# Performance work log

Hardware: AMD Instinct MI355X
Metric: run time of the kernel (lower is better)

The kernel has to match this reference:

```python
import jax, jax.numpy as jnp
import numpy as np

B, T, F = 2048, 96, 32
H = 1024
G_EMB = 16
LSTM_IN = F + 11 + 1 + G_EMB  # 60


def _lstm_cell(x, h, c, W_ih, W_hh, b):
    g = x @ W_ih.T + h @ W_hh.T + b
    i, f, gg, o = jnp.split(g, 4, axis=-1)  # torch gate order: i, f, g, o
    c_new = jax.nn.sigmoid(f) * c + jax.nn.sigmoid(i) * jnp.tanh(gg)
    h_new = jax.nn.sigmoid(o) * jnp.tanh(c_new)
    return h_new, c_new


def setup_inputs() -> dict:
    key = jax.random.key(0)
    ks = jax.random.split(key, 26)
    s = 1.0 / np.sqrt(H)
    inp = {
        "dec_known": jax.random.normal(ks[0], (B, T, F), jnp.float32),
        "target_y": jax.random.normal(ks[1], (B, T, 1), jnp.float32),
        "enc_h": jax.random.normal(ks[2], (2, B, H), jnp.float32),
        "enc_c": jax.random.normal(ks[3], (2, B, H), jnp.float32),
        "last_enc_consumption": jax.random.normal(ks[4], (B, 1), jnp.float32),
        "group_ids": jax.random.randint(ks[5], (B,), 0, 1000),
        "cat_province": jax.random.randint(ks[6], (B,), 0, 13),
        "cat_customer_type": jax.random.randint(ks[7], (B,), 0, 2),
        "cat_price_type": jax.random.randint(ks[8], (B,), 0, 5),
        "cat_consumption_level": jax.random.randint(ks[9], (B,), 0, 3),
        # learned parameters
        "group_emb": jax.random.normal(ks[10], (1000, G_EMB), jnp.float32),
        "emb_province": jax.random.normal(ks[11], (13, 4), jnp.float32),
        "emb_customer_type": jax.random.normal(ks[12], (2, 2), jnp.float32),
        "emb_price_type": jax.random.normal(ks[13], (5, 3), jnp.float32),
        "emb_consumption_level": jax.random.normal(ks[14], (3, 2), jnp.float32),
        "W_ih0": jax.random.normal(ks[15], (4 * H, LSTM_IN), jnp.float32) * s,
        "W_hh0": jax.random.normal(ks[16], (4 * H, H), jnp.float32) * s,
        "b0": jax.random.normal(ks[17], (4 * H,), jnp.float32) * s,
        "W_ih1": jax.random.normal(ks[18], (4 * H, H), jnp.float32) * s,
        "W_hh1": jax.random.normal(ks[19], (4 * H, H), jnp.float32) * s,
        "b1": jax.random.normal(ks[20], (4 * H,), jnp.float32) * s,
        "W_proj": jax.random.normal(ks[21], (1, H), jnp.float32) * s,
        "b_proj": jnp.zeros((1,), jnp.float32),
    }
    return inp


def reference(dec_known, target_y, enc_h, enc_c, last_enc_consumption,
              group_ids, cat_province, cat_customer_type, cat_price_type,
              cat_consumption_level, group_emb, emb_province, emb_customer_type,
              emb_price_type, emb_consumption_level, W_ih0, W_hh0, b0,
              W_ih1, W_hh1, b1, W_proj, b_proj):
    b, t, _ = dec_known.shape
    # static per-sample features (categorical + group embeddings)
    cat_emb = jnp.concatenate([
        emb_province[cat_province], emb_customer_type[cat_customer_type],
        emb_price_type[cat_price_type], emb_consumption_level[cat_consumption_level],
    ], axis=-1)  # [B, 11]
    group_vec = group_emb[group_ids]  # [B, 16]
    static = jnp.concatenate([cat_emb, group_vec], axis=-1)  # [B, 27]
    # teacher_forcing_ratio = 1.0 => prev_y is last_enc_consumption then target_y shifted
    prev_y = jnp.concatenate([last_enc_consumption[:, None, :], target_y[:, :-1, :]], axis=1)  # [B,T,1]
    x = jnp.concatenate([
        prev_y, dec_known,
        jnp.broadcast_to(static[:, None, :], (b, t, static.shape[-1])),
    ], axis=-1)  # [B, T, 60]

    def step(carry, x_t):
        h1, c1, h2, c2 = carry
        h1, c1 = _lstm_cell(x_t, h1, c1, W_ih0, W_hh0, b0)
        h2, c2 = _lstm_cell(h1, h2, c2, W_ih1, W_hh1, b1)
        return (h1, c1, h2, c2), h2

    init = (enc_h[0], enc_c[0], enc_h[1], enc_c[1])
    _, hs = jax.lax.scan(step, init, jnp.swapaxes(x, 0, 1))  # hs: [T, B, H]
    y = jnp.einsum('tbh,oh->bto', hs, W_proj) + b_proj  # [B, T, 1]
    return y
```

## Files before the change

### kernel.cpp

```cpp
#include <hip/hip_runtime.h>
#include <hip/hip_bf16.h>
#include <stdint.h>


#define BB  2048
#define TT  96
#define NG  4096
#define KL1 1088
#define KL2 2048

typedef __bf16 bf16;
typedef __bf16 bf16x8 __attribute__((ext_vector_type(8)));
typedef float  f32x4  __attribute__((ext_vector_type(4)));

__device__ __forceinline__ float sigm(float x) { return 1.0f / (1.0f + __expf(-x)); }

__device__ __forceinline__ void gload16(const bf16* g, bf16* l) {
  __builtin_amdgcn_global_load_lds((const __attribute__((address_space(1))) void*)g,
                                   (__attribute__((address_space(3))) void*)l, 16, 0, 0);
}


__global__ __launch_bounds__(256) void build_w0(const float* __restrict__ Wih0,
                                                const float* __restrict__ Whh0,
                                                bf16* __restrict__ W0) {
  int idx = blockIdx.x * 256 + threadIdx.x;
  if (idx >= NG * KL1) return;
  int np = idx / KL1, k = idx % KL1;
  int n = (np & 3) * 1024 + (np >> 2);
  float v;
  if (k < 60)       v = Wih0[n * 60 + k];
  else if (k < 64)  v = 0.0f;
  else              v = Whh0[n * 1024 + (k - 64)];
  W0[idx] = (bf16)v;
}

__global__ __launch_bounds__(256) void build_w1(const float* __restrict__ Wih1,
                                                const float* __restrict__ Whh1,
                                                bf16* __restrict__ W1) {
  int idx = blockIdx.x * 256 + threadIdx.x;
  if (idx >= NG * KL2) return;
  int np = idx >> 11, k = idx & 2047;
  int n = (np & 3) * 1024 + (np >> 2);
  float v = (k < 1024) ? Wih1[n * 1024 + k] : Whh1[n * 1024 + (k - 1024)];
  W1[idx] = (bf16)v;
}

__global__ __launch_bounds__(256) void perm_bias(const float* __restrict__ b0,
                                                 const float* __restrict__ b1,
                                                 float* __restrict__ b0p,
                                                 float* __restrict__ b1p) {
  int idx = blockIdx.x * 256 + threadIdx.x;
  if (idx >= NG) return;
  int n = (idx & 3) * 1024 + (idx >> 2);
  b0p[idx] = b0[n];
  b1p[idx] = b1[n];
}

__global__ __launch_bounds__(256) void build_x(
    const float* __restrict__ dec, const float* __restrict__ ty, const float* __restrict__ lec,
    const int* __restrict__ gid, const int* __restrict__ cp, const int* __restrict__ cct,
    const int* __restrict__ cpt, const int* __restrict__ ccl,
    const float* __restrict__ gemb, const float* __restrict__ ep, const float* __restrict__ ect,
    const float* __restrict__ ept, const float* __restrict__ ecl,
    bf16* __restrict__ X) {
  int idx = blockIdx.x * 256 + threadIdx.x;
  if (idx >= BB * TT) return;
  int b = idx / TT, t = idx % TT;
  bf16* x = X + (size_t)idx * 64;
  x[0] = (bf16)((t == 0) ? lec[b] : ty[b * TT + t - 1]);
  const float* d = dec + (size_t)idx * 32;
  #pragma unroll
  for (int k = 0; k < 32; ++k) x[1 + k] = (bf16)d[k];
  const float* e;
  e = ep  + cp[b]  * 4;  for (int j = 0; j < 4;  ++j) x[33 + j] = (bf16)e[j];
  e = ect + cct[b] * 2;  for (int j = 0; j < 2;  ++j) x[37 + j] = (bf16)e[j];
  e = ept + cpt[b] * 3;  for (int j = 0; j < 3;  ++j) x[39 + j] = (bf16)e[j];
  e = ecl + ccl[b] * 2;  for (int j = 0; j < 2;  ++j) x[42 + j] = (bf16)e[j];
  e = gemb + gid[b] * 16; for (int j = 0; j < 16; ++j) x[44 + j] = (bf16)e[j];
  for (int j = 60; j < 64; ++j) x[j] = (bf16)0.0f;
}

__global__ __launch_bounds__(256) void init_state(const float* __restrict__ enc_h,
                                                  const float* __restrict__ enc_c,
                                                  bf16* __restrict__ H1b,
                                                  bf16* __restrict__ H2b,
                                                  float* __restrict__ c1t,
                                                  float* __restrict__ c2t) {
  int idx = blockIdx.x * 256 + threadIdx.x;
  if (idx >= BB * 1024) return;
  int b = idx >> 10, h = idx & 1023;
  H1b[idx] = (bf16)enc_h[idx];
  H2b[idx] = (bf16)enc_h[(size_t)BB * 1024 + idx];
  c1t[(size_t)h * BB + b] = enc_c[idx];
  c2t[(size_t)h * BB + b] = enc_c[(size_t)BB * 1024 + idx];
}


template <int MODE>
__device__ __forceinline__ void gemm_cell_body(
    int vb, int t,
    const bf16* __restrict__ P0, const bf16* __restrict__ P1,
    const bf16* __restrict__ Wt, const float* __restrict__ bperm,
    float* __restrict__ ct, bf16* __restrict__ Hout,
    const float* __restrict__ wp, const float* __restrict__ bp,
    float* __restrict__ y,
    bf16* As, bf16* Ws) {
  constexpr int KT = (MODE == 0) ? KL1 : KL2;
  constexpr int NT = KT / 32;

  int tid = threadIdx.x;
  int swz = (vb & 7) * 64 + (vb >> 3);
  int tm = (swz & 15) << 7;
  int tn = (swz >> 4) << 7;
  int lane = tid & 63;
  int w = tid >> 6;
  int wg = (w & 1) << 6;
  int wb = (w >> 1) << 6;

  f32x4 acc[4][4];
  #pragma unroll
  for (int mw = 0; mw < 4; ++mw)
    #pragma unroll
    for (int nb = 0; nb < 4; ++nb) acc[mw][nb] = (f32x4){0.f, 0.f, 0.f, 0.f};

  int r0 = tid >> 2, r1 = (256 + tid) >> 2;
  int kc0 = (((tid & 3) ^ (r0 & 3)) << 3);
  int kc1 = (((tid & 3) ^ (r1 & 3)) << 3);
  int dst0 = (tid & ~63) * 8;
  int dst1 = 2048 + dst0;

  auto aptr = [&](int row, int gk) -> const bf16* {
    if constexpr (MODE == 0) {
      return (gk < 64) ? (P0 + ((size_t)(tm + row) * TT + t) * 64 + gk)
                       : (P1 + (size_t)(tm + row) * 1024 + (gk - 64));
    } else {
      return (gk < 1024) ? (P0 + (size_t)(tm + row) * 1024 + gk)
                         : (P1 + (size_t)(tm + row) * 1024 + (gk - 1024));
    }
  };

  gload16(aptr(r0, kc0), As + dst0);
  gload16(aptr(r1, kc1), As + dst1);
  gload16(Wt + (size_t)(tn + r0) * KT + kc0, Ws + dst0);
  gload16(Wt + (size_t)(tn + r1) * KT + kc1, Ws + dst1);
  __syncthreads();

  int lrow = lane & 15;
  int klocal = (((lane >> 4) ^ (lane & 3)) << 3);

  for (int kt = 0; kt < NT; ++kt) {
    int cur = (kt & 1) << 12;
    if (kt + 1 < NT) {
      int nxt = 4096 - cur;
      int gk0 = (kt + 1) * 32 + kc0, gk1 = (kt + 1) * 32 + kc1;
      gload16(aptr(r0, gk0), As + nxt + dst0);
      gload16(aptr(r1, gk1), As + nxt + dst1);
      gload16(Wt + (size_t)(tn + r0) * KT + gk0, Ws + nxt + dst0);
      gload16(Wt + (size_t)(tn + r1) * KT + gk1, Ws + nxt + dst1);
    }
    __builtin_amdgcn_sched_barrier(0);

    bf16x8 af[4], wf[4];
    #pragma unroll
    for (int nb = 0; nb < 4; ++nb)
      af[nb] = *reinterpret_cast<const bf16x8*>(&As[cur + (wb + nb * 16 + lrow) * 32 + klocal]);
    #pragma unroll
    for (int mw = 0; mw < 4; ++mw)
      wf[mw] = *reinterpret_cast<const bf16x8*>(&Ws[cur + (wg + mw * 16 + lrow) * 32 + klocal]);
    #pragma unroll
    for (int mw = 0; mw < 4; ++mw)
      #pragma unroll
      for (int nb = 0; nb < 4; ++nb)
        acc[mw][nb] = __builtin_amdgcn_mfma_f32_16x16x32_bf16(wf[mw], af[nb], acc[mw][nb], 0, 0, 0);

    __syncthreads();
  }

  bf16* hst = As + w * 1024;
  int u = lane >> 4;
  int bl = lane & 15;
  int hwave = (tn + wg) >> 2;
  float yp[4] = {0.f, 0.f, 0.f, 0.f};

  #pragma unroll
  for (int mw = 0; mw < 4; ++mw) {
    int hg = hwave + mw * 4 + u;
    f32x4 bv = *reinterpret_cast<const f32x4*>(&bperm[hg * 4]);
    float wph = 0.f;
    if constexpr (MODE == 1) wph = wp[hg];
    #pragma unroll
    for (int nb = 0; nb < 4; ++nb) {
      int bg = tm + wb + nb * 16 + bl;
      float gi = acc[mw][nb][0] + bv[0];
      float gf = acc[mw][nb][1] + bv[1];
      float gg = acc[mw][nb][2] + bv[2];
      float go = acc[mw][nb][3] + bv[3];
      float* cp_ = ct + (size_t)hg * BB + bg;
      float c = *cp_;
      float cn = sigm(gf) * c + sigm(gi) * tanhf(gg);
      float hn = sigm(go) * tanhf(cn);
      *cp_ = cn;
      hst[(nb * 16 + bl) * 16 + mw * 4 + u] = (bf16)hn;
      if constexpr (MODE == 1) yp[nb] += hn * wph;
    }
  }

  asm volatile("s_waitcnt lgkmcnt(0)" ::: "memory");
  __builtin_amdgcn_sched_barrier(0);

  #pragma unroll
  for (int q = 0; q < 2; ++q) {
    int chunk = q * 64 + lane;
    int bl2 = chunk >> 1, half = chunk & 1;
    bf16x8 v = *reinterpret_cast<const bf16x8*>(&hst[bl2 * 16 + half * 8]);
    int bg = tm + wb + bl2;
    *reinterpret_cast<bf16x8*>(&Hout[(size_t)bg * 1024 + hwave + half * 8]) = v;
  }

  if constexpr (MODE == 1) {
    #pragma unroll
    for (int nb = 0; nb < 4; ++nb) {
      float s = yp[nb];
      s += __shfl_xor(s, 16);
      s += __shfl_xor(s, 32);
      if (lane < 16)
        atomicAdd(&y[(size_t)(tm + wb + nb * 16 + lane) * TT + t], s);
    }
  } else {
    if (tn == 0 && tid < 128) y[(size_t)(tm + tid) * TT + t] = bp[0];
  }
}

__global__ __launch_bounds__(256, 4) void step_kernel(
    const bf16* __restrict__ H1in, const bf16* __restrict__ H2in,
    bf16* __restrict__ H1out, bf16* __restrict__ H2out,
    const bf16* __restrict__ X,
    const bf16* __restrict__ W0, const bf16* __restrict__ W1,
    const float* __restrict__ b0p, const float* __restrict__ b1p,
    float* __restrict__ c1t, float* __restrict__ c2t,
    const float* __restrict__ wp, const float* __restrict__ bp,
    float* __restrict__ y, int t2, int only_l1) {
  __shared__ alignas(16) bf16 As[2 * 4096];
  __shared__ alignas(16) bf16 Ws[2 * 4096];
  int bid = (int)blockIdx.x;
  if (only_l1 || bid >= 512) {
    int vb = only_l1 ? bid : bid - 512;
    int t1 = t2 + 1;
    if (t1 >= TT) return;
    gemm_cell_body<0>(vb, t1, X, H1in, W0, b0p, c1t, H1out, nullptr, bp, y, As, Ws);
  } else {
    gemm_cell_body<1>(bid, t2, H1in, H2in, W1, b1p, c2t, H2out, wp, nullptr, y, As, Ws);
  }
}


extern "C" void kernel_launch(void* const* d_in, const int* in_sizes, int n_in,
                              void* d_out, int out_size, void* d_ws, size_t ws_size,
                              hipStream_t stream) {
  const float* dec   = (const float*)d_in[0];
  const float* ty    = (const float*)d_in[1];
  const float* enc_h = (const float*)d_in[2];
  const float* enc_c = (const float*)d_in[3];
  const float* lec   = (const float*)d_in[4];
  const int*   gid   = (const int*)d_in[5];
  const int*   cp    = (const int*)d_in[6];
  const int*   cct   = (const int*)d_in[7];
  const int*   cpt   = (const int*)d_in[8];
  const int*   ccl   = (const int*)d_in[9];
  const float* gemb  = (const float*)d_in[10];
  const float* ep    = (const float*)d_in[11];
  const float* ect   = (const float*)d_in[12];
  const float* ept   = (const float*)d_in[13];
  const float* ecl   = (const float*)d_in[14];
  const float* Wih0  = (const float*)d_in[15];
  const float* Whh0  = (const float*)d_in[16];
  const float* b0    = (const float*)d_in[17];
  const float* Wih1  = (const float*)d_in[18];
  const float* Whh1  = (const float*)d_in[19];
  const float* b1    = (const float*)d_in[20];
  const float* wp    = (const float*)d_in[21];
  const float* bp    = (const float*)d_in[22];
  float* y = (float*)d_out;

  char* ws = (char*)d_ws;
  bf16* W0    = (bf16*)ws;  ws += (size_t)NG * KL1 * 2;
  bf16* W1    = (bf16*)ws;  ws += (size_t)NG * KL2 * 2;
  bf16* X     = (bf16*)ws;  ws += (size_t)BB * TT * 64 * 2;
  bf16* H1a   = (bf16*)ws;  ws += (size_t)BB * 1024 * 2;
  bf16* H1b   = (bf16*)ws;  ws += (size_t)BB * 1024 * 2;
  bf16* H2a   = (bf16*)ws;  ws += (size_t)BB * 1024 * 2;
  bf16* H2b   = (bf16*)ws;  ws += (size_t)BB * 1024 * 2;
  float* c1t  = (float*)ws; ws += (size_t)BB * 1024 * 4;
  float* c2t  = (float*)ws; ws += (size_t)BB * 1024 * 4;
  float* b0p  = (float*)ws; ws += (size_t)NG * 4;
  float* b1p  = (float*)ws; ws += (size_t)NG * 4;

  build_w0<<<(NG * KL1 + 255) / 256, 256, 0, stream>>>(Wih0, Whh0, W0);
  build_w1<<<(NG * KL2 + 255) / 256, 256, 0, stream>>>(Wih1, Whh1, W1);
  perm_bias<<<NG / 256, 256, 0, stream>>>(b0, b1, b0p, b1p);
  build_x<<<(BB * TT + 255) / 256, 256, 0, stream>>>(dec, ty, lec, gid, cp, cct, cpt, ccl,
                                                     gemb, ep, ect, ept, ecl, X);
  init_state<<<(BB * 1024) / 256, 256, 0, stream>>>(enc_h, enc_c, H1b, H2b, c1t, c2t);

  step_kernel<<<512, 256, 0, stream>>>(H1b, nullptr, H1a, nullptr, X, W0, W1,
                                       b0p, b1p, c1t, c2t, wp, bp, y, -1, 1);
  for (int t = 0; t < TT; ++t) {
    bf16* h1i = (t & 1) ? H1b : H1a;
    bf16* h1o = (t & 1) ? H1a : H1b;
    bf16* h2i = (t & 1) ? H2a : H2b;
    bf16* h2o = (t & 1) ? H2b : H2a;
    step_kernel<<<1024, 256, 0, stream>>>(h1i, h2i, h1o, h2o, X, W0, W1,
                                          b0p, b1p, c1t, c2t, wp, bp, y, t, 0);
  }
}
```

Before: 7.137 ms.

## Prefetch two K-tiles ahead with explicit waitcnt barriers and new LDS swizzle

Restructures the GEMM main loop so that global-to-LDS loads for tile kt+2 are issued right after the current tile's fragments are read into registers. Synchronisation uses manual vmcnt/lgkmcnt waits and raw barriers, which gives loads a deeper prefetch distance and drops the trailing __syncthreads. The LDS XOR swizzle now keys on row>>1, to cut bank conflicts for the 16-row fragment reads. MFMA sections run at raised wave priority. This adds fragile hand-coded wait counts that must match the number of outstanding loads.

Result: no change. 7.236 ms (+1.4%).

```diff
diff --git a/kernel.cpp b/kernel.cpp
--- a/kernel.cpp
+++ b/kernel.cpp
@@ -125,8 +125,8 @@
     for (int nb = 0; nb < 4; ++nb) acc[mw][nb] = (f32x4){0.f, 0.f, 0.f, 0.f};
 
   int r0 = tid >> 2, r1 = (256 + tid) >> 2;
-  int kc0 = (((tid & 3) ^ (r0 & 3)) << 3);
-  int kc1 = (((tid & 3) ^ (r1 & 3)) << 3);
+  int kc0 = (((tid & 3) ^ ((r0 >> 1) & 3)) << 3);
+  int kc1 = (((tid & 3) ^ ((r1 >> 1) & 3)) << 3);
   int dst0 = (tid & ~63) * 8;
   int dst1 = 2048 + dst0;
 
@@ -139,26 +139,25 @@
                          : (P1 + (size_t)(tm + row) * 1024 + (gk - 1024));
     }
   };
-
-  gload16(aptr(r0, kc0), As + dst0);
-  gload16(aptr(r1, kc1), As + dst1);
-  gload16(Wt + (size_t)(tn + r0) * KT + kc0, Ws + dst0);
-  gload16(Wt + (size_t)(tn + r1) * KT + kc1, Ws + dst1);
-  __syncthreads();
+  auto stage = [&](int kt, int off) {
+    int gk0 = kt * 32 + kc0, gk1 = kt * 32 + kc1;
+    gload16(aptr(r0, gk0), As + off + dst0);
+    gload16(aptr(r1, gk1), As + off + dst1);
+    gload16(Wt + (size_t)(tn + r0) * KT + gk0, Ws + off + dst0);
+    gload16(Wt + (size_t)(tn + r1) * KT + gk1, Ws + off + dst1);
+  };
+
+  stage(0, 0);
+  stage(1, 4096);
 
   int lrow = lane & 15;
-  int klocal = (((lane >> 4) ^ (lane & 3)) << 3);
+  int klocal = ((((lane >> 4) ^ (lrow >> 1)) & 3) << 3);
 
   for (int kt = 0; kt < NT; ++kt) {
     int cur = (kt & 1) << 12;
-    if (kt + 1 < NT) {
-      int nxt = 4096 - cur;
-      int gk0 = (kt + 1) * 32 + kc0, gk1 = (kt + 1) * 32 + kc1;
-      gload16(aptr(r0, gk0), As + nxt + dst0);
-      gload16(aptr(r1, gk1), As + nxt + dst1);
-      gload16(Wt + (size_t)(tn + r0) * KT + gk0, Ws + nxt + dst0);
-      gload16(Wt + (size_t)(tn + r1) * KT + gk1, Ws + nxt + dst1);
-    }
+    if (kt + 1 < NT) { asm volatile("s_waitcnt vmcnt(4)" ::: "memory"); }
+    else             { asm volatile("s_waitcnt vmcnt(0)" ::: "memory"); }
+    __builtin_amdgcn_s_barrier();
     __builtin_amdgcn_sched_barrier(0);
 
     bf16x8 af[4], wf[4];
@@ -168,13 +167,21 @@
     #pragma unroll
     for (int mw = 0; mw < 4; ++mw)
       wf[mw] = *reinterpret_cast<const bf16x8*>(&Ws[cur + (wg + mw * 16 + lrow) * 32 + klocal]);
+
+    asm volatile("s_waitcnt lgkmcnt(0)" ::: "memory");
+    __builtin_amdgcn_sched_barrier(0);
+    __builtin_amdgcn_s_barrier();
+    __builtin_amdgcn_sched_barrier(0);
+
+    if (kt + 2 < NT) stage(kt + 2, cur);
+
+    __builtin_amdgcn_s_setprio(1);
     #pragma unroll
     for (int mw = 0; mw < 4; ++mw)
       #pragma unroll
       for (int nb = 0; nb < 4; ++nb)
         acc[mw][nb] = __builtin_amdgcn_mfma_f32_16x16x32_bf16(wf[mw], af[nb], acc[mw][nb], 0, 0, 0);
-
-    __syncthreads();
+    __builtin_amdgcn_s_setprio(0);
   }
 
   bf16* hst = As + w * 1024;
```

## Switch LSTM step GEMM to 256x256 tiles with 8-wave ping-pong pipeline

Applied to the files above, without the earlier changes.

Replaces the 128x128 tile, 4-wave step kernel with a 256x256 tile, 512-thread kernel using BK=64, double-buffered LDS staging interleaved with MFMA phases under explicit barriers and priority hints. X is re-laid out time-major so each step reads a contiguous slice, and block-to-tile mapping interleaves layer-1 and layer-2 tiles. Larger tiles raise arithmetic intensity and cut global traffic. The cost is only 256 blocks per step, which may underfill the 256 CUs, plus higher register pressure from 32 accumulators per lane.

Result: slower. 7.856 ms (+10.1%).

```diff
diff --git a/kernel.cpp b/kernel.cpp
--- a/kernel.cpp
+++ b/kernel.cpp
@@ -19,6 +19,11 @@
   __builtin_amdgcn_global_load_lds((const __attribute__((address_space(1))) void*)g,
                                    (__attribute__((address_space(3))) void*)l, 16, 0, 0);
 }
+
+#define SB()  __builtin_amdgcn_sched_barrier(0)
+#define BAR() __builtin_amdgcn_s_barrier()
+#define WAITV0() asm volatile("s_waitcnt vmcnt(0)" ::: "memory")
+#define WAITL0() asm volatile("s_waitcnt lgkmcnt(0)" ::: "memory")
 
 
 __global__ __launch_bounds__(256) void build_w0(const float* __restrict__ Wih0,
@@ -57,19 +62,19 @@
   b1p[idx] = b1[n];
 }
 
-__global__ __launch_bounds__(256) void build_x(
+__global__ __launch_bounds__(256) void build_x2(
     const float* __restrict__ dec, const float* __restrict__ ty, const float* __restrict__ lec,
     const int* __restrict__ gid, const int* __restrict__ cp, const int* __restrict__ cct,
     const int* __restrict__ cpt, const int* __restrict__ ccl,
     const float* __restrict__ gemb, const float* __restrict__ ep, const float* __restrict__ ect,
     const float* __restrict__ ept, const float* __restrict__ ecl,
-    bf16* __restrict__ X) {
+    bf16* __restrict__ X2) {
   int idx = blockIdx.x * 256 + threadIdx.x;
   if (idx >= BB * TT) return;
-  int b = idx / TT, t = idx % TT;
-  bf16* x = X + (size_t)idx * 64;
+  int t = idx >> 11, b = idx & 2047;
+  bf16* x = X2 + (size_t)idx * 64;
   x[0] = (bf16)((t == 0) ? lec[b] : ty[b * TT + t - 1]);
-  const float* d = dec + (size_t)idx * 32;
+  const float* d = dec + ((size_t)b * TT + t) * 32;
   #pragma unroll
   for (int k = 0; k < 32; ++k) x[1 + k] = (bf16)d[k];
   const float* e;
@@ -98,159 +103,216 @@
 
 
 template <int MODE>
-__device__ __forceinline__ void gemm_cell_body(
-    int vb, int t,
+__device__ __forceinline__ void gemm_body(
+    int tm, int tn, int t,
     const bf16* __restrict__ P0, const bf16* __restrict__ P1,
     const bf16* __restrict__ Wt, const float* __restrict__ bperm,
     float* __restrict__ ct, bf16* __restrict__ Hout,
     const float* __restrict__ wp, const float* __restrict__ bp,
     float* __restrict__ y,
-    bf16* As, bf16* Ws) {
+    bf16* Al, bf16* Wl)
+{
   constexpr int KT = (MODE == 0) ? KL1 : KL2;
-  constexpr int NT = KT / 32;
-
-  int tid = threadIdx.x;
-  int swz = (vb & 7) * 64 + (vb >> 3);
-  int tm = (swz & 15) << 7;
-  int tn = (swz >> 4) << 7;
-  int lane = tid & 63;
-  int w = tid >> 6;
-  int wg = (w & 1) << 6;
-  int wb = (w >> 1) << 6;
-
-  f32x4 acc[4][4];
+  constexpr int NT = KT / 64;
+
+  const int tid = threadIdx.x;
+  const int lane = tid & 63, w = tid >> 6;
+  const int l15 = lane & 15, u = lane >> 4;
+  const int wq = w & 3, wbh = w >> 2;
+
+  f32x4 acc[8][4];
   #pragma unroll
-  for (int mw = 0; mw < 4; ++mw)
-    #pragma unroll
-    for (int nb = 0; nb < 4; ++nb) acc[mw][nb] = (f32x4){0.f, 0.f, 0.f, 0.f};
-
-  int r0 = tid >> 2, r1 = (256 + tid) >> 2;
-  int kc0 = (((tid & 3) ^ (r0 & 3)) << 3);
-  int kc1 = (((tid & 3) ^ (r1 & 3)) << 3);
-  int dst0 = (tid & ~63) * 8;
-  int dst1 = 2048 + dst0;
-
-  auto aptr = [&](int row, int gk) -> const bf16* {
+  for (int i = 0; i < 8; ++i)
+    #pragma unroll
+    for (int j = 0; j < 4; ++j) acc[i][j] = (f32x4){0.f, 0.f, 0.f, 0.f};
+
+  const int srow = w * 8 + (lane >> 3);
+  const int kx   = (lane & 7) ^ (srow & 7);
+  const int dA   = w * 512 + lane * 8;
+  const int jx0 = ((u     ) ^ (l15 & 7)) << 3;
+  const int jx1 = ((4 + u ) ^ (l15 & 7)) << 3;
+
+  auto asrc = [&](int row, int kt) -> const bf16* {
     if constexpr (MODE == 0) {
-      return (gk < 64) ? (P0 + ((size_t)(tm + row) * TT + t) * 64 + gk)
-                       : (P1 + (size_t)(tm + row) * 1024 + (gk - 64));
+      if (kt == 0) return P0 + (size_t)(tm + row) * 64 + kx * 8;
+      return P1 + (size_t)(tm + row) * 1024 + (kt - 1) * 64 + kx * 8;
     } else {
-      return (gk < 1024) ? (P0 + (size_t)(tm + row) * 1024 + gk)
-                         : (P1 + (size_t)(tm + row) * 1024 + (gk - 1024));
+      if (kt < 16) return P0 + (size_t)(tm + row) * 1024 + kt * 64 + kx * 8;
+      return P1 + (size_t)(tm + row) * 1024 + (kt - 16) * 64 + kx * 8;
     }
   };
-
-  gload16(aptr(r0, kc0), As + dst0);
-  gload16(aptr(r1, kc1), As + dst1);
-  gload16(Wt + (size_t)(tn + r0) * KT + kc0, Ws + dst0);
-  gload16(Wt + (size_t)(tn + r1) * KT + kc1, Ws + dst1);
-  __syncthreads();
-
-  int lrow = lane & 15;
-  int klocal = (((lane >> 4) ^ (lane & 3)) << 3);
+  auto stageA = [&](int buf, int half, int kt) {
+    bf16* base = Al + (buf * 2 + half) * 8192;
+    gload16(asrc(half * 128 + srow, kt),      base + dA);
+    gload16(asrc(half * 128 + srow + 64, kt), base + dA + 4096);
+  };
+  auto stageW = [&](int buf, int half, int kt) {
+    bf16* base = Wl + (buf * 2 + half) * 8192;
+    const bf16* g0 = Wt + (size_t)(tn + half * 128 + srow) * KT + kt * 64 + kx * 8;
+    const bf16* g1 = Wt + (size_t)(tn + half * 128 + srow + 64) * KT + kt * 64 + kx * 8;
+    gload16(g0, base + dA);
+    gload16(g1, base + dA + 4096);
+  };
+  auto rdA = [&](int buf, int bf, int ks) -> bf16x8 {
+    return *reinterpret_cast<const bf16x8*>(
+        Al + (buf * 2 + wbh) * 8192 + (bf * 16 + l15) * 64 + (ks ? jx1 : jx0));
+  };
+  auto rdW = [&](int buf, int gf, int ks) -> bf16x8 {
+    return *reinterpret_cast<const bf16x8*>(
+        Wl + (buf * 2 + (wq >> 1)) * 8192 + ((wq & 1) * 64 + gf * 16 + l15) * 64 + (ks ? jx1 : jx0));
+  };
+
+  stageA(0, 0, 0); stageA(0, 1, 0); stageW(0, 0, 0); stageW(0, 1, 0);
+
+  bf16x8 a_[8], w0_[4], w1_[4];
 
   for (int kt = 0; kt < NT; ++kt) {
-    int cur = (kt & 1) << 12;
-    if (kt + 1 < NT) {
-      int nxt = 4096 - cur;
-      int gk0 = (kt + 1) * 32 + kc0, gk1 = (kt + 1) * 32 + kc1;
-      gload16(aptr(r0, gk0), As + nxt + dst0);
-      gload16(aptr(r1, gk1), As + nxt + dst1);
-      gload16(Wt + (size_t)(tn + r0) * KT + gk0, Ws + nxt + dst0);
-      gload16(Wt + (size_t)(tn + r1) * KT + gk1, Ws + nxt + dst1);
-    }
-    __builtin_amdgcn_sched_barrier(0);
-
-    bf16x8 af[4], wf[4];
-    #pragma unroll
-    for (int nb = 0; nb < 4; ++nb)
-      af[nb] = *reinterpret_cast<const bf16x8*>(&As[cur + (wb + nb * 16 + lrow) * 32 + klocal]);
-    #pragma unroll
-    for (int mw = 0; mw < 4; ++mw)
-      wf[mw] = *reinterpret_cast<const bf16x8*>(&Ws[cur + (wg + mw * 16 + lrow) * 32 + klocal]);
-    #pragma unroll
-    for (int mw = 0; mw < 4; ++mw)
+    const int buf = kt & 1, nbuf = buf ^ 1;
+    const bool pre = (kt + 1 < NT);
+
+    WAITV0(); SB(); BAR(); SB();
+    if (pre) { stageA(nbuf, 0, kt + 1); stageA(nbuf, 1, kt + 1); }
+
+    #pragma unroll
+    for (int bf = 0; bf < 4; ++bf) { a_[bf * 2] = rdA(buf, bf, 0); a_[bf * 2 + 1] = rdA(buf, bf, 1); }
+    #pragma unroll
+    for (int g = 0; g < 2; ++g) { w0_[g * 2] = rdW(buf, g, 0); w0_[g * 2 + 1] = rdW(buf, g, 1); }
+    if (pre) stageW(nbuf, 0, kt + 1);
+    SB(); BAR();
+    WAITL0(); SB();
+    __builtin_amdgcn_s_setprio(1);
+    #pragma unroll
+    for (int bf = 0; bf < 4; ++bf)
       #pragma unroll
-      for (int nb = 0; nb < 4; ++nb)
-        acc[mw][nb] = __builtin_amdgcn_mfma_f32_16x16x32_bf16(wf[mw], af[nb], acc[mw][nb], 0, 0, 0);
-
-    __syncthreads();
-  }
-
-  bf16* hst = As + w * 1024;
-  int u = lane >> 4;
-  int bl = lane & 15;
-  int hwave = (tn + wg) >> 2;
-  float yp[4] = {0.f, 0.f, 0.f, 0.f};
+      for (int g = 0; g < 2; ++g)
+        #pragma unroll
+        for (int ks = 0; ks < 2; ++ks)
+          acc[bf][g] = __builtin_amdgcn_mfma_f32_16x16x32_bf16(w0_[g * 2 + ks], a_[bf * 2 + ks], acc[bf][g], 0, 0, 0);
+    __builtin_amdgcn_s_setprio(0);
+    SB(); BAR();
+
+    #pragma unroll
+    for (int g = 0; g < 2; ++g) { w1_[g * 2] = rdW(buf, 2 + g, 0); w1_[g * 2 + 1] = rdW(buf, 2 + g, 1); }
+    if (pre) stageW(nbuf, 1, kt + 1);
+    SB(); BAR();
+    WAITL0(); SB();
+    __builtin_amdgcn_s_setprio(1);
+    #pragma unroll
+    for (int bf = 0; bf < 4; ++bf)
+      #pragma unroll
+      for (int g = 0; g < 2; ++g)
+        #pragma unroll
+        for (int ks = 0; ks < 2; ++ks)
+          acc[bf][2 + g] = __builtin_amdgcn_mfma_f32_16x16x32_bf16(w1_[g * 2 + ks], a_[bf * 2 + ks], acc[bf][2 + g], 0, 0, 0);
+    __builtin_amdgcn_s_setprio(0);
+    SB(); BAR();
+
+    #pragma unroll
+    for (int bf = 0; bf < 4; ++bf) { a_[bf * 2] = rdA(buf, 4 + bf, 0); a_[bf * 2 + 1] = rdA(buf, 4 + bf, 1); }
+    SB(); BAR();
+    WAITL0(); SB();
+    __builtin_amdgcn_s_setprio(1);
+    #pragma unroll
+    for (int bf = 0; bf < 4; ++bf)
+      #pragma unroll
+      for (int g = 0; g < 2; ++g)
+        #pragma unroll
+        for (int ks = 0; ks < 2; ++ks)
+          acc[4 + bf][2 + g] = __builtin_amdgcn_mfma_f32_16x16x32_bf16(w1_[g * 2 + ks], a_[bf * 2 + ks], acc[4 + bf][2 + g], 0, 0, 0);
+    __builtin_amdgcn_s_setprio(0);
+    SB(); BAR();
+
+    __builtin_amdgcn_s_setprio(1);
+    #pragma unroll
+    for (int bf = 0; bf < 4; ++bf)
+      #pragma unroll
+      for (int g = 0; g < 2; ++g)
+        #pragma unroll
+        for (int ks = 0; ks < 2; ++ks)
+          acc[4 + bf][g] = __builtin_amdgcn_mfma_f32_16x16x32_bf16(w0_[g * 2 + ks], a_[bf * 2 + ks], acc[4 + bf][g], 0, 0, 0);
+    __builtin_amdgcn_s_setprio(0);
+  }
+
+  SB(); BAR(); SB();
+
+  bf16* hst = Al + w * 3072;
+  const int hb = (tn >> 2) + wq * 16;
+  const int bgb = tm + wbh * 128;
+  float yp[8] = {0.f, 0.f, 0.f, 0.f, 0.f, 0.f, 0.f, 0.f};
 
   #pragma unroll
-  for (int mw = 0; mw < 4; ++mw) {
-    int hg = hwave + mw * 4 + u;
+  for (int gf = 0; gf < 4; ++gf) {
+    int hg = hb + gf * 4 + u;
     f32x4 bv = *reinterpret_cast<const f32x4*>(&bperm[hg * 4]);
     float wph = 0.f;
     if constexpr (MODE == 1) wph = wp[hg];
     #pragma unroll
-    for (int nb = 0; nb < 4; ++nb) {
-      int bg = tm + wb + nb * 16 + bl;
-      float gi = acc[mw][nb][0] + bv[0];
-      float gf = acc[mw][nb][1] + bv[1];
-      float gg = acc[mw][nb][2] + bv[2];
-      float go = acc[mw][nb][3] + bv[3];
+    for (int bf = 0; bf < 8; ++bf) {
+      int bg = bgb + bf * 16 + l15;
+      float gi = acc[bf][gf][0] + bv[0];
+      float gf_ = acc[bf][gf][1] + bv[1];
+      float gg = acc[bf][gf][2] + bv[2];
+      float go = acc[bf][gf][3] + bv[3];
       float* cp_ = ct + (size_t)hg * BB + bg;
       float c = *cp_;
-      float cn = sigm(gf) * c + sigm(gi) * tanhf(gg);
+      float cn = sigm(gf_) * c + sigm(gi) * tanhf(gg);
       float hn = sigm(go) * tanhf(cn);
       *cp_ = cn;
-      hst[(nb * 16 + bl) * 16 + mw * 4 + u] = (bf16)hn;
-      if constexpr (MODE == 1) yp[nb] += hn * wph;
+      hst[(bf * 16 + l15) * 24 + gf * 4 + u] = (bf16)hn;
+      if constexpr (MODE == 1) yp[bf] += hn * wph;
     }
   }
 
-  asm volatile("s_waitcnt lgkmcnt(0)" ::: "memory");
-  __builtin_amdgcn_sched_barrier(0);
+  WAITL0(); SB();
 
   #pragma unroll
-  for (int q = 0; q < 2; ++q) {
+  for (int q = 0; q < 4; ++q) {
     int chunk = q * 64 + lane;
-    int bl2 = chunk >> 1, half = chunk & 1;
-    bf16x8 v = *reinterpret_cast<const bf16x8*>(&hst[bl2 * 16 + half * 8]);
-    int bg = tm + wb + bl2;
-    *reinterpret_cast<bf16x8*>(&Hout[(size_t)bg * 1024 + hwave + half * 8]) = v;
+    int row = chunk >> 1, half8 = chunk & 1;
+    bf16x8 v = *reinterpret_cast<const bf16x8*>(&hst[row * 24 + half8 * 8]);
+    *reinterpret_cast<bf16x8*>(&Hout[(size_t)(bgb + row) * 1024 + hb + half8 * 8]) = v;
   }
 
   if constexpr (MODE == 1) {
     #pragma unroll
-    for (int nb = 0; nb < 4; ++nb) {
-      float s = yp[nb];
+    for (int bf = 0; bf < 8; ++bf) {
+      float s = yp[bf];
       s += __shfl_xor(s, 16);
       s += __shfl_xor(s, 32);
       if (lane < 16)
-        atomicAdd(&y[(size_t)(tm + wb + nb * 16 + lane) * TT + t], s);
+        atomicAdd(&y[(size_t)(bgb + bf * 16 + lane) * TT + t], s);
     }
   } else {
-    if (tn == 0 && tid < 128) y[(size_t)(tm + tid) * TT + t] = bp[0];
-  }
-}
-
-__global__ __launch_bounds__(256, 4) void step_kernel(
+    if (tn == 0 && tid < 256) y[(size_t)(tm + tid) * TT + t] = bp[0];
+  }
+}
+
+__global__ __launch_bounds__(512, 2) void step256(
     const bf16* __restrict__ H1in, const bf16* __restrict__ H2in,
     bf16* __restrict__ H1out, bf16* __restrict__ H2out,
-    const bf16* __restrict__ X,
+    const bf16* __restrict__ X2,
     const bf16* __restrict__ W0, const bf16* __restrict__ W1,
     const float* __restrict__ b0p, const float* __restrict__ b1p,
     float* __restrict__ c1t, float* __restrict__ c2t,
     const float* __restrict__ wp, const float* __restrict__ bp,
-    float* __restrict__ y, int t2, int only_l1) {
-  __shared__ alignas(16) bf16 As[2 * 4096];
-  __shared__ alignas(16) bf16 Ws[2 * 4096];
+    float* __restrict__ y, int t2, int all_l1) {
+  __shared__ alignas(16) bf16 Al[32768];
+  __shared__ alignas(16) bf16 Wl[32768];
   int bid = (int)blockIdx.x;
-  if (only_l1 || bid >= 512) {
-    int vb = only_l1 ? bid : bid - 512;
+  int mode, tmx, tnx;
+  if (all_l1) { mode = 0; tmx = bid >> 4; tnx = bid & 15; }
+  else {
+    int x = bid & 7, i = bid >> 3;
+    mode = i & 1; tmx = i >> 2; tnx = x * 2 + ((i >> 1) & 1);
+  }
+  if (mode == 0) {
     int t1 = t2 + 1;
     if (t1 >= TT) return;
-    gemm_cell_body<0>(vb, t1, X, H1in, W0, b0p, c1t, H1out, nullptr, bp, y, As, Ws);
+    gemm_body<0>(tmx * 256, tnx * 256, t1, X2 + (size_t)t1 * 2048 * 64, H1in,
+                 W0, b0p, c1t, H1out, nullptr, bp, y, Al, Wl);
   } else {
-    gemm_cell_body<1>(bid, t2, H1in, H2in, W1, b1p, c2t, H2out, wp, nullptr, y, As, Ws);
+    gemm_body<1>(tmx * 256, tnx * 256, t2, H1in, H2in,
+                 W1, b1p, c2t, H2out, wp, nullptr, y, Al, Wl);
   }
 }
 
@@ -286,7 +348,7 @@
   char* ws = (char*)d_ws;
   bf16* W0    = (bf16*)ws;  ws += (size_t)NG * KL1 * 2;
   bf16* W1    = (bf16*)ws;  ws += (size_t)NG * KL2 * 2;
-  bf16* X     = (bf16*)ws;  ws += (size_t)BB * TT * 64 * 2;
+  bf16* X2    = (bf16*)ws;  ws += (size_t)BB * TT * 64 * 2;
   bf16* H1a   = (bf16*)ws;  ws += (size_t)BB * 1024 * 2;
   bf16* H1b   = (bf16*)ws;  ws += (size_t)BB * 1024 * 2;
   bf16* H2a   = (bf16*)ws;  ws += (size_t)BB * 1024 * 2;
@@ -299,18 +361,18 @@
   build_w0<<<(NG * KL1 + 255) / 256, 256, 0, stream>>>(Wih0, Whh0, W0);
   build_w1<<<(NG * KL2 + 255) / 256, 256, 0, stream>>>(Wih1, Whh1, W1);
   perm_bias<<<NG / 256, 256, 0, stream>>>(b0, b1, b0p, b1p);
-  build_x<<<(BB * TT + 255) / 256, 256, 0, stream>>>(dec, ty, lec, gid, cp, cct, cpt, ccl,
-                                                     gemb, ep, ect, ept, ecl, X);
+  build_x2<<<(BB * TT + 255) / 256, 256, 0, stream>>>(dec, ty, lec, gid, cp, cct, cpt, ccl,
+                                                      gemb, ep, ect, ept, ecl, X2);
   init_state<<<(BB * 1024) / 256, 256, 0, stream>>>(enc_h, enc_c, H1b, H2b, c1t, c2t);
 
-  step_kernel<<<512, 256, 0, stream>>>(H1b, nullptr, H1a, nullptr, X, W0, W1,
-                                       b0p, b1p, c1t, c2t, wp, bp, y, -1, 1);
+  step256<<<128, 512, 0, stream>>>(H1b, nullptr, H1a, nullptr, X2, W0, W1,
+                                   b0p, b1p, c1t, c2t, wp, bp, y, -1, 1);
   for (int t = 0; t < TT; ++t) {
     bf16* h1i = (t & 1) ? H1b : H1a;
     bf16* h1o = (t & 1) ? H1a : H1b;
     bf16* h2i = (t & 1) ? H2a : H2b;
     bf16* h2o = (t & 1) ? H2b : H2a;
-    step_kernel<<<1024, 256, 0, stream>>>(h1i, h2i, h1o, h2o, X, W0, W1,
-                                          b0p, b1p, c1t, c2t, wp, bp, y, t, 0);
-  }
-}
+    step256<<<256, 512, 0, stream>>>(h1i, h2i, h1o, h2o, X2, W0, W1,
+                                     b0p, b1p, c1t, c2t, wp, bp, y, t, 0);
+  }
+}
```
